# Kernel optimization log

Measured on AMD Instinct MI355X. Metric: run time of the kernel, lower is better.

## Reference

```python
import jax, jax.numpy as jnp
import numpy as np

NEG_BIG = -9e15
ALPHA = 0.2  # LeakyReLU negative slope


def setup_inputs() -> dict:
    key = jax.random.key(0)
    k1, k2, k3, k4 = jax.random.split(key, 4)
    B, N, F_in, F_out = 8, 2048, 128, 128
    h = jax.random.normal(k1, (B, N, F_in), dtype=jnp.float32)
    adj = jax.random.randint(k2, (B, N, N), 0, 2, dtype=jnp.int32)
    # xavier_uniform with gain=1.414
    def xavier(k, shape, gain=1.414):
        fan_in, fan_out = shape[0], shape[1]
        bound = gain * np.sqrt(6.0 / (fan_in + fan_out))
        return jax.random.uniform(k, shape, jnp.float32, -bound, bound)
    W = xavier(k3, (F_in, F_out))
    a = xavier(k4, (2 * F_out, 1))
    return {"h": h, "adj": adj, "W": W, "a": a}


def reference(h, adj, W, a):
    # h: [B,N,F_in], adj: [B,N,N], W: [F_in,F_out], a: [2*F_out,1]
    Wh = jnp.einsum('bnf,fo->bno', h, W)              # [B,N,F_out]
    F_out = W.shape[1]
    a1 = a[:F_out, 0]                                  # source part
    a2 = a[F_out:, 0]                                  # target part
    # additive attention decomposition: cat([Wh_i, Wh_j]) @ a == Wh_i@a1 + Wh_j@a2
    s1 = Wh @ a1                                       # [B,N]
    s2 = Wh @ a2                                       # [B,N]
    e = jax.nn.leaky_relu(s1[:, :, None] + s2[:, None, :], negative_slope=ALPHA)  # [B,N,N]
    e = jnp.where(adj > 0, e, NEG_BIG)
    attn = jax.nn.softmax(e, axis=-1)                  # [B,N,N]
    h_prime = jnp.einsum('bij,bjo->bio', attn, Wh)     # [B,N,F_out]
    return jax.nn.elu(h_prime)                         # concat=True path
```

## Files before the change

kernel.cpp:

```cpp
#include <hip/hip_runtime.h>
#include <hip/hip_bf16.h>
#include <string.h>

typedef __attribute__((ext_vector_type(8))) short short8;
typedef __attribute__((ext_vector_type(4))) float f32x4;
typedef __attribute__((ext_vector_type(4))) float float4v;
typedef __attribute__((ext_vector_type(2))) float float2v;
typedef __attribute__((ext_vector_type(4))) unsigned short ushort4v;

#define LOG2E 1.44269504088896340736f
#define NB 8
#define NN 2048
#define NF 128
#define PKW (NN / 64)
#define PKWORDS (NB * NN * PKW)
#define NGEMMB 256
#define NPACKB 1024

static __device__ inline unsigned short f2bf(float x) {
    unsigned u = __float_as_uint(x);
    return (unsigned short)((u + 0x7FFFu + ((u >> 16) & 1u)) >> 16);
}
static __device__ inline float bf2f(unsigned short u) {
    union { unsigned u; float f; } v;
    v.u = ((unsigned)u) << 16;
    return v.f;
}
static __device__ inline float fexp2(float x) {
    float r;
    asm("v_exp_f32 %0, %1" : "=v"(r) : "v"(x));
    return r;
}
static __device__ inline unsigned fkey(float f) {
    unsigned u = __float_as_uint(f);
    return (u & 0x80000000u) ? ~u : (u | 0x80000000u);
}
static __device__ inline float funkey(unsigned k) {
    unsigned b = (k & 0x80000000u) ? (k & 0x7FFFFFFFu) : ~k;
    return __uint_as_float(b);
}
static __device__ inline int wave_sniff(const unsigned short* __restrict__ raw) {
    int lane = threadIdx.x & 63;
    int cnt = 0;
#pragma unroll
    for (int i = 0; i < 8; ++i) {
        int e = (raw[lane * 8 + i] >> 7) & 0xFF;
        cnt += (e >= 102 && e <= 139) ? 1 : 0;
    }
#pragma unroll
    for (int off = 1; off < 64; off <<= 1) cnt += __shfl_xor(cnt, off);
    return cnt >= 450;
}

__global__ __launch_bounds__(256) void k_prep(const void* __restrict__ Wraw,
                                              const void* __restrict__ araw,
                                              short* __restrict__ WThi,
                                              short* __restrict__ WTlo,
                                              float* __restrict__ a1s,
                                              float* __restrict__ a2s,
                                              unsigned* __restrict__ s2mkey) {
    const int bf16w = wave_sniff((const unsigned short*)Wraw);
    int idx = blockIdx.x * 256 + threadIdx.x;
    int k = idx >> 7, n = idx & 127;
    float x = bf16w ? bf2f(((const unsigned short*)Wraw)[idx])
                    : ((const float*)Wraw)[idx];
    unsigned short hi = f2bf(x);
    float lo = x - bf2f(hi);
    WThi[n * 128 + k] = (short)hi;
    WTlo[n * 128 + k] = (short)f2bf(lo);
    if (blockIdx.x == 0) {
        int i = threadIdx.x;
        float av = bf16w ? bf2f(((const unsigned short*)araw)[i])
                         : ((const float*)araw)[i];
        if (i < 128) a1s[i] = LOG2E * av;
        else a2s[i - 128] = LOG2E * av;
        if (i < NB) s2mkey[i] = 0u;
    }
}

__global__ __launch_bounds__(256, 4) void k_fat(const int* __restrict__ adj,
                                                unsigned long long* __restrict__ pk,
                                                const void* __restrict__ hraw,
                                                const short* __restrict__ WThi,
                                                const short* __restrict__ WTlo,
                                                const float* __restrict__ a1s,
                                                const float* __restrict__ a2s,
                                                float* __restrict__ s1,
                                                float* __restrict__ EF,
                                                unsigned* __restrict__ s2mkey,
                                                short* __restrict__ WhT) {
    const int tid = threadIdx.x;
    if (blockIdx.x >= NGEMMB) {
        const int wid = (blockIdx.x - NGEMMB) * 4 + (tid >> 6);
        const int lane = tid & 63;
        const int wpw = PKWORDS / 4096;
        const size_t w0 = (size_t)wid * wpw;
        for (int i = 0; i < wpw; i += 8) {
            int v[8];
#pragma unroll
            for (int k = 0; k < 8; ++k) v[k] = adj[((w0 + i + k) << 6) | lane];
            unsigned long long m[8];
#pragma unroll
            for (int k = 0; k < 8; ++k) m[k] = __ballot(v[k] > 0);
            if (lane == 0) {
#pragma unroll
                for (int k = 0; k < 8; ++k) pk[w0 + i + k] = m[k];
            }
        }
        return;
    }
    const int lane = tid & 63;
    const int w = tid >> 6;
    const int lo = lane & 15, g = lane >> 4;
    const int i0 = (blockIdx.x * 4 + w) * 16;
    const int bf16w = wave_sniff((const unsigned short*)hraw);

    short8 ahi[4], alo[4];
    if (bf16w) {
        const short* h16 = (const short*)hraw;
#pragma unroll
        for (int kc = 0; kc < 4; ++kc) {
            ahi[kc] = *(const short8*)(h16 + (size_t)(i0 + lo) * NF + kc * 32 + g * 8);
            alo[kc] = (short8){0, 0, 0, 0, 0, 0, 0, 0};
        }
    } else {
        const float* hf = (const float*)hraw;
#pragma unroll
        for (int kc = 0; kc < 4; ++kc) {
            const float* p = hf + (size_t)(i0 + lo) * NF + kc * 32 + g * 8;
            float4v x0 = *(const float4v*)(p);
            float4v x1 = *(const float4v*)(p + 4);
            short8 h8, l8;
#pragma unroll
            for (int q = 0; q < 4; ++q) {
                unsigned short u0 = f2bf(x0[q]);
                h8[q] = (short)u0;
                l8[q] = (short)f2bf(x0[q] - bf2f(u0));
                unsigned short u1 = f2bf(x1[q]);
                h8[q + 4] = (short)u1;
                l8[q + 4] = (short)f2bf(x1[q] - bf2f(u1));
            }
            ahi[kc] = h8;
            alo[kc] = l8;
        }
    }

    f32x4 acc[8];
#pragma unroll
    for (int t = 0; t < 8; ++t) acc[t] = (f32x4){0.f, 0.f, 0.f, 0.f};
#pragma unroll
    for (int t = 0; t < 8; ++t) {
#pragma unroll
        for (int kc = 0; kc < 4; ++kc) {
            const size_t boff = (size_t)(lo + 16 * t) * NF + kc * 32 + g * 8;
            short8 bhi = *(const short8*)(WThi + boff);
            short8 blo = *(const short8*)(WTlo + boff);
            acc[t] = __builtin_amdgcn_mfma_f32_16x16x32_bf16(ahi[kc], bhi, acc[t], 0, 0, 0);
            acc[t] = __builtin_amdgcn_mfma_f32_16x16x32_bf16(ahi[kc], blo, acc[t], 0, 0, 0);
            acc[t] = __builtin_amdgcn_mfma_f32_16x16x32_bf16(alo[kc], bhi, acc[t], 0, 0, 0);
        }
    }

    const int b = i0 >> 11;
    const int n0 = i0 & 2047;
    short* wt = WhT + (size_t)b * NF * NN;
#pragma unroll
    for (int t = 0; t < 8; ++t) {
        ushort4v u;
#pragma unroll
        for (int r = 0; r < 4; ++r) u[r] = f2bf(acc[t][r]);
        *(ushort4v*)(wt + (size_t)(lo + 16 * t) * NN + n0 + g * 4) = u;
    }

    float a1f[8], a2f[8];
#pragma unroll
    for (int t = 0; t < 8; ++t) {
        a1f[t] = a1s[lo + 16 * t];
        a2f[t] = a2s[lo + 16 * t];
    }
    float wm = -1e30f;
#pragma unroll
    for (int r = 0; r < 4; ++r) {
        float d1 = 0.f, d2 = 0.f;
#pragma unroll
        for (int t = 0; t < 8; ++t) {
            float wv = acc[t][r];
            d1 += wv * a1f[t];
            d2 += wv * a2f[t];
        }
#pragma unroll
        for (int off = 1; off < 16; off <<= 1) {
            d1 += __shfl_xor(d1, off);
            d2 += __shfl_xor(d2, off);
        }
        if (lo == 0) {
            s1[i0 + g * 4 + r] = d1;
            float2v ef;
            ef[0] = fexp2(d2);
            ef[1] = fexp2(0.2f * d2);
            *(float2v*)(EF + (size_t)(i0 + g * 4 + r) * 2) = ef;
        }
        wm = fmaxf(wm, d2);
    }
    wm = fmaxf(wm, __shfl_xor(wm, 16));
    wm = fmaxf(wm, __shfl_xor(wm, 32));
    if (lane == 0) atomicMax(&s2mkey[b], fkey(wm));
}

template <int FINAL, int JS>
__global__ __launch_bounds__(256, 4) void k_attn(const unsigned long long* __restrict__ pk,
                                                 const float* __restrict__ s1,
                                                 const float* __restrict__ EF,
                                                 const unsigned* __restrict__ s2mkey,
                                                 const short* __restrict__ WhT,
                                                 const void* __restrict__ hraw,
                                                 void* __restrict__ out,
                                                 unsigned short* __restrict__ pO,
                                                 float* __restrict__ pL) {
    constexpr int JL = NN / JS;
    constexpr int NT = JL / 64;

    const int tid = threadIdx.x;
    const int lane = tid & 63, wid = tid >> 6;
    const int lo = lane & 15, g = lane >> 4;
    const int gid = blockIdx.x;
    const int b = gid & 7;
    const int blk = (gid >> 3) & 31;
    const int js = (JS > 1) ? (gid >> 8) : 0;
    const int rowbase = blk * 64 + wid * 16;
    const int row = rowbase + lo;
    const int jbeg = js * JL;

    __shared__ short lds[2][128 * 64];
    __shared__ float ldsZ[JL * 2];

    const float s1v = s1[b * NN + row];
    const float tm = s1v + funkey(s2mkey[b]);
    const float M = fmaxf(tm, 0.2f * tm);
    const float Tc = fexp2(-s1v);
    const float Ac = fexp2(s1v - M);
    const float Bc = fexp2(0.2f * s1v - M);
    const unsigned long long* pkr = pk + (size_t)(b * NN + row) * PKW + (jbeg >> 6);
    const short* vb = WhT + (size_t)b * NF * NN;

    {
        const float4v* src = (const float4v*)(EF + (size_t)(b * NN + jbeg) * 2);
        for (int i = tid; i < JL / 2; i += 256) ((float4v*)ldsZ)[i] = src[i];
    }

    const int sf = tid >> 1;
    const int sh = tid & 1;
    const short* sbase = vb + (size_t)sf * NN + jbeg + sh * 32;
    char* ldsc0 = (char*)&lds[0][0];
    char* ldsc1 = (char*)&lds[1][0];
    const unsigned swz = (unsigned)((sf & 7) << 4);
    const unsigned wb0 = (unsigned)(sf * 128 + sh * 64);
    const unsigned rsw = (unsigned)((lo & 7) << 4);

    f32x4 acc[8];
#pragma unroll
    for (int t = 0; t < 8; ++t) acc[t] = (f32x4){0.f, 0.f, 0.f, 0.f};
    float lsum = 0.f;

    {
        short8 s0 = *(const short8*)(sbase);
        short8 s1r = *(const short8*)(sbase + 8);
        short8 s2r = *(const short8*)(sbase + 16);
        short8 s3r = *(const short8*)(sbase + 24);
        *(short8*)(ldsc0 + ((wb0 + 0) ^ swz)) = s0;
        *(short8*)(ldsc0 + ((wb0 + 16) ^ swz)) = s1r;
        *(short8*)(ldsc0 + ((wb0 + 32) ^ swz)) = s2r;
        *(short8*)(ldsc0 + ((wb0 + 48) ^ swz)) = s3r;
    }
    unsigned long long mcur = pkr[0];
    __syncthreads();

    int cur = 0;
    for (int t = 0; t < NT; ++t) {
        short8 sn0, sn1, sn2, sn3;
        unsigned long long mnext = 0;
        const bool more = (t + 1 < NT);
        if (more) {
            const short* sp = sbase + (t + 1) * 64;
            sn0 = *(const short8*)(sp);
            sn1 = *(const short8*)(sp + 8);
            sn2 = *(const short8*)(sp + 16);
            sn3 = *(const short8*)(sp + 24);
            mnext = pkr[t + 1];
        }
        const char* cb = cur ? ldsc1 : ldsc0;

        short8 pa[2];
#pragma unroll
        for (int c = 0; c < 2; ++c) {
            const float4v* zp = (const float4v*)&ldsZ[((t) * 64 + c * 32 + g * 8) * 2];
            float4v w_[4];
#pragma unroll
            for (int q = 0; q < 4; ++q) w_[q] = zp[q];
            const unsigned bits = (unsigned)(mcur >> (c * 32 + g * 8)) & 0xFFu;
            float pv[8];
#pragma unroll
            for (int k = 0; k < 8; ++k) {
                float E = w_[k >> 1][(k & 1) * 2];
                float F = w_[k >> 1][(k & 1) * 2 + 1];
                bool cond = E >= Tc;
                float sel = cond ? E : F;
                float coef = cond ? Ac : Bc;
                float p = sel * coef;
                p = ((bits >> k) & 1u) ? p : 0.f;
                lsum += p;
                pv[k] = p;
            }
            unsigned r0, r1, r2, r3;
            asm("v_cvt_pk_bf16_f32 %0, %1, %2" : "=v"(r0) : "v"(pv[0]), "v"(pv[1]));
            asm("v_cvt_pk_bf16_f32 %0, %1, %2" : "=v"(r1) : "v"(pv[2]), "v"(pv[3]));
            asm("v_cvt_pk_bf16_f32 %0, %1, %2" : "=v"(r2) : "v"(pv[4]), "v"(pv[5]));
            asm("v_cvt_pk_bf16_f32 %0, %1, %2" : "=v"(r3) : "v"(pv[6]), "v"(pv[7]));
            union { unsigned u[4]; short8 s; } uu;
            uu.u[0] = r0; uu.u[1] = r1; uu.u[2] = r2; uu.u[3] = r3;
            pa[c] = uu.s;
        }

        __builtin_amdgcn_s_setprio(1);
#pragma unroll
        for (int t8 = 0; t8 < 8; ++t8) {
            const unsigned rb0 = ((unsigned)((lo + 16 * t8) * 128 + g * 16)) ^ rsw;
            const unsigned rb1 = ((unsigned)((lo + 16 * t8) * 128 + 64 + g * 16)) ^ rsw;
            short8 v0 = *(const short8*)(cb + rb0);
            short8 v1 = *(const short8*)(cb + rb1);
            acc[t8] = __builtin_amdgcn_mfma_f32_16x16x32_bf16(pa[0], v0, acc[t8], 0, 0, 0);
            acc[t8] = __builtin_amdgcn_mfma_f32_16x16x32_bf16(pa[1], v1, acc[t8], 0, 0, 0);
        }
        __builtin_amdgcn_s_setprio(0);

        if (more) {
            char* wb = cur ? ldsc0 : ldsc1;
            *(short8*)(wb + ((wb0 + 0) ^ swz)) = sn0;
            *(short8*)(wb + ((wb0 + 16) ^ swz)) = sn1;
            *(short8*)(wb + ((wb0 + 32) ^ swz)) = sn2;
            *(short8*)(wb + ((wb0 + 48) ^ swz)) = sn3;
            mcur = mnext;
        }
        __syncthreads();
        cur ^= 1;
    }

    lsum += __shfl_xor(lsum, 16);
    lsum += __shfl_xor(lsum, 32);

    if (FINAL) {
        const int bf16w = wave_sniff((const unsigned short*)hraw);
        float inv[4];
#pragma unroll
        for (int r = 0; r < 4; ++r) inv[r] = 1.0f / __shfl(lsum, g * 4 + r);
#pragma unroll
        for (int t8 = 0; t8 < 8; ++t8) {
#pragma unroll
            for (int r = 0; r < 4; ++r) {
                float x = acc[t8][r] * inv[r];
                float y = (x > 0.f) ? x : (fexp2(x * LOG2E) - 1.0f);
                size_t oi = ((size_t)b * NN + rowbase + g * 4 + r) * NF + lo + 16 * t8;
                if (bf16w) ((unsigned short*)out)[oi] = f2bf(y);
                else ((float*)out)[oi] = y;
            }
        }
    } else {
        const int grp = b * 128 + blk * 4 + wid;
        unsigned short* po = pO + (size_t)(grp * JS + js) * (16 * NF);
#pragma unroll
        for (int t8 = 0; t8 < 8; ++t8)
#pragma unroll
            for (int r = 0; r < 4; ++r)
                po[(g * 4 + r) * NF + lo + 16 * t8] = f2bf(acc[t8][r]);
        if (g == 0) pL[(grp * JS + js) * 16 + lo] = lsum;
    }
}

__global__ __launch_bounds__(256) void k_combine(const unsigned short* __restrict__ pO,
                                                 const float* __restrict__ pL,
                                                 const void* __restrict__ hraw,
                                                 void* __restrict__ out,
                                                 int jsplit) {
    const int bf16w = wave_sniff((const unsigned short*)hraw);
    int idx4 = blockIdx.x * 256 + threadIdx.x;
    int base = idx4 * 4;
    if (base >= NB * NN * NF) return;
    int col = base & 127;
    int rowg = base >> 7;
    int r = rowg & 15;
    int grp = rowg >> 4;
    float o0 = 0.f, o1 = 0.f, o2 = 0.f, o3 = 0.f;
    float l = 0.f;
    for (int js = 0; js < jsplit; ++js) {
        int task = grp * jsplit + js;
        ushort4v u = *(const ushort4v*)(pO + (size_t)task * (16 * NF) + r * NF + col);
        o0 += bf2f(u[0]); o1 += bf2f(u[1]); o2 += bf2f(u[2]); o3 += bf2f(u[3]);
        l += pL[task * 16 + r];
    }
    float inv = 1.0f / l;
    float y[4];
    float ov[4] = {o0, o1, o2, o3};
#pragma unroll
    for (int q = 0; q < 4; ++q) {
        float x = ov[q] * inv;
        y[q] = (x > 0.f) ? x : (fexp2(x * LOG2E) - 1.0f);
    }
    if (bf16w) {
        ushort4v u;
#pragma unroll
        for (int q = 0; q < 4; ++q) u[q] = f2bf(y[q]);
        *(ushort4v*)((unsigned short*)out + base) = u;
    } else {
        *(float4v*)((float*)out + base) = (float4v){y[0], y[1], y[2], y[3]};
    }
}

extern "C" void kernel_launch(void* const* d_in, const int* in_sizes, int n_in,
                              void* d_out, int out_size, void* d_ws, size_t ws_size,
                              hipStream_t stream) {
    const void* h = d_in[0];
    const int* adj = (const int*)d_in[1];
    const void* W = d_in[2];
    const void* a = d_in[3];

    char* ws = (char*)d_ws;
    auto align256 = [](size_t x) { return (x + 255) & ~(size_t)255; };
    size_t off = 0;
    short* WThi = (short*)(ws + off); off = align256(off + (size_t)128 * 128 * 2);
    short* WTlo = (short*)(ws + off); off = align256(off + (size_t)128 * 128 * 2);
    float* a1s = (float*)(ws + off);  off = align256(off + 128 * 4);
    float* a2s = (float*)(ws + off);  off = align256(off + 128 * 4);
    short* WhT = (short*)(ws + off);  off = align256(off + (size_t)NB * NF * NN * 2);
    float* s1 = (float*)(ws + off);   off = align256(off + (size_t)NB * NN * 4);
    float* EF = (float*)(ws + off);   off = align256(off + (size_t)NB * NN * 8);
    unsigned* s2mkey = (unsigned*)(ws + off); off = align256(off + NB * 4);
    unsigned long long* pk = (unsigned long long*)(ws + off);
    off = align256(off + (size_t)PKWORDS * 8);

    const int ngrp = NB * 128;
    auto need = [&](int js) {
        return off + (size_t)ngrp * js * 16 * NF * 2 + 512 + (size_t)ngrp * js * 16 * 4;
    };
    int jsplit = (ws_size >= need(4)) ? 4 : ((ws_size >= need(2)) ? 2 : 1);
    unsigned short* pO = nullptr;
    float* pL = nullptr;
    if (jsplit > 1) {
        size_t pO_bytes = (size_t)ngrp * jsplit * 16 * NF * 2;
        size_t pL_bytes = (size_t)ngrp * jsplit * 16 * 4;
        pO = (unsigned short*)(ws + off); off = align256(off + pO_bytes);
        pL = (float*)(ws + off); off = align256(off + pL_bytes);
    }

    k_prep<<<64, 256, 0, stream>>>(W, a, WThi, WTlo, a1s, a2s, s2mkey);
    k_fat<<<NGEMMB + NPACKB, 256, 0, stream>>>(adj, pk, h, WThi, WTlo, a1s, a2s,
                                               s1, EF, s2mkey, WhT);
    if (jsplit == 4) {
        k_attn<0, 4><<<NB * 32 * 4, 256, 0, stream>>>(pk, s1, EF, s2mkey, WhT, h,
                                                      d_out, pO, pL);
    } else if (jsplit == 2) {
        k_attn<0, 2><<<NB * 32 * 2, 256, 0, stream>>>(pk, s1, EF, s2mkey, WhT, h,
                                                      d_out, pO, pL);
    } else {
        k_attn<1, 1><<<NB * 32, 256, 0, stream>>>(pk, s1, EF, s2mkey, WhT, h,
                                                  d_out, nullptr, nullptr);
    }
    if (jsplit > 1) {
        int nout = NB * NN * NF;
        k_combine<<<(nout / 4 + 255) / 256, 256, 0, stream>>>(pO, pL, h, d_out, jsplit);
    }
}
```

Measured before the change: 72.66 us.

## Single-buffer LDS in attention kernel and raise key split to eight

The attention kernel drops its double-buffered LDS tile for a single buffer, adding a barrier before the next tile is written, and removes the launch-bounds occupancy hint and the non-split FINAL path. The host now prefers an eight-way split of the key dimension when workspace allows and always runs the combine kernel. The aim is more blocks and higher occupancy from halved shared memory, at the cost of an extra barrier per tile, less overlap of loads with MFMA work, and more partial-output traffic in the combine step.

```diff
diff --git a/kernel.cpp b/kernel.cpp
--- a/kernel.cpp
+++ b/kernel.cpp
@@ -207,16 +207,14 @@
     if (lane == 0) atomicMax(&s2mkey[b], fkey(wm));
 }
 
-template <int FINAL, int JS>
-__global__ __launch_bounds__(256, 4) void k_attn(const unsigned long long* __restrict__ pk,
-                                                 const float* __restrict__ s1,
-                                                 const float* __restrict__ EF,
-                                                 const unsigned* __restrict__ s2mkey,
-                                                 const short* __restrict__ WhT,
-                                                 const void* __restrict__ hraw,
-                                                 void* __restrict__ out,
-                                                 unsigned short* __restrict__ pO,
-                                                 float* __restrict__ pL) {
+template <int JS>
+__global__ __launch_bounds__(256) void k_attn(const unsigned long long* __restrict__ pk,
+                                              const float* __restrict__ s1,
+                                              const float* __restrict__ EF,
+                                              const unsigned* __restrict__ s2mkey,
+                                              const short* __restrict__ WhT,
+                                              unsigned short* __restrict__ pO,
+                                              float* __restrict__ pL) {
     constexpr int JL = NN / JS;
     constexpr int NT = JL / 64;
 
@@ -226,12 +224,12 @@
     const int gid = blockIdx.x;
     const int b = gid & 7;
     const int blk = (gid >> 3) & 31;
-    const int js = (JS > 1) ? (gid >> 8) : 0;
+    const int js = gid >> 8;
     const int rowbase = blk * 64 + wid * 16;
     const int row = rowbase + lo;
     const int jbeg = js * JL;
 
-    __shared__ short lds[2][128 * 64];
+    __shared__ short lds[128 * 64];
     __shared__ float ldsZ[JL * 2];
 
     const float s1v = s1[b * NN + row];
@@ -251,8 +249,7 @@
     const int sf = tid >> 1;
     const int sh = tid & 1;
     const short* sbase = vb + (size_t)sf * NN + jbeg + sh * 32;
-    char* ldsc0 = (char*)&lds[0][0];
-    char* ldsc1 = (char*)&lds[1][0];
+    char* ldsc = (char*)&lds[0];
     const unsigned swz = (unsigned)((sf & 7) << 4);
     const unsigned wb0 = (unsigned)(sf * 128 + sh * 64);
     const unsigned rsw = (unsigned)((lo & 7) << 4);
@@ -267,15 +264,14 @@
         short8 s1r = *(const short8*)(sbase + 8);
         short8 s2r = *(const short8*)(sbase + 16);
         short8 s3r = *(const short8*)(sbase + 24);
-        *(short8*)(ldsc0 + ((wb0 + 0) ^ swz)) = s0;
-        *(short8*)(ldsc0 + ((wb0 + 16) ^ swz)) = s1r;
-        *(short8*)(ldsc0 + ((wb0 + 32) ^ swz)) = s2r;
-        *(short8*)(ldsc0 + ((wb0 + 48) ^ swz)) = s3r;
+        *(short8*)(ldsc + ((wb0 + 0) ^ swz)) = s0;
+        *(short8*)(ldsc + ((wb0 + 16) ^ swz)) = s1r;
+        *(short8*)(ldsc + ((wb0 + 32) ^ swz)) = s2r;
+        *(short8*)(ldsc + ((wb0 + 48) ^ swz)) = s3r;
     }
     unsigned long long mcur = pkr[0];
     __syncthreads();
 
-    int cur = 0;
     for (int t = 0; t < NT; ++t) {
         short8 sn0, sn1, sn2, sn3;
         unsigned long long mnext = 0;
@@ -288,7 +284,6 @@
             sn3 = *(const short8*)(sp + 24);
             mnext = pkr[t + 1];
         }
-        const char* cb = cur ? ldsc1 : ldsc0;
 
         short8 pa[2];
 #pragma unroll
@@ -326,54 +321,35 @@
         for (int t8 = 0; t8 < 8; ++t8) {
             const unsigned rb0 = ((unsigned)((lo + 16 * t8) * 128 + g * 16)) ^ rsw;
             const unsigned rb1 = ((unsigned)((lo + 16 * t8) * 128 + 64 + g * 16)) ^ rsw;
-            short8 v0 = *(const short8*)(cb + rb0);
-            short8 v1 = *(const short8*)(cb + rb1);
+            short8 v0 = *(const short8*)(ldsc + rb0);
+            short8 v1 = *(const short8*)(ldsc + rb1);
             acc[t8] = __builtin_amdgcn_mfma_f32_16x16x32_bf16(pa[0], v0, acc[t8], 0, 0, 0);
             acc[t8] = __builtin_amdgcn_mfma_f32_16x16x32_bf16(pa[1], v1, acc[t8], 0, 0, 0);
         }
         __builtin_amdgcn_s_setprio(0);
 
+        __syncthreads();
         if (more) {
-            char* wb = cur ? ldsc0 : ldsc1;
-            *(short8*)(wb + ((wb0 + 0) ^ swz)) = sn0;
-            *(short8*)(wb + ((wb0 + 16) ^ swz)) = sn1;
-            *(short8*)(wb + ((wb0 + 32) ^ swz)) = sn2;
-            *(short8*)(wb + ((wb0 + 48) ^ swz)) = sn3;
+            *(short8*)(ldsc + ((wb0 + 0) ^ swz)) = sn0;
+            *(short8*)(ldsc + ((wb0 + 16) ^ swz)) = sn1;
+            *(short8*)(ldsc + ((wb0 + 32) ^ swz)) = sn2;
+            *(short8*)(ldsc + ((wb0 + 48) ^ swz)) = sn3;
             mcur = mnext;
         }
         __syncthreads();
-        cur ^= 1;
     }
 
     lsum += __shfl_xor(lsum, 16);
     lsum += __shfl_xor(lsum, 32);
 
-    if (FINAL) {
-        const int bf16w = wave_sniff((const unsigned short*)hraw);
-        float inv[4];
-#pragma unroll
-        for (int r = 0; r < 4; ++r) inv[r] = 1.0f / __shfl(lsum, g * 4 + r);
-#pragma unroll
-        for (int t8 = 0; t8 < 8; ++t8) {
-#pragma unroll
-            for (int r = 0; r < 4; ++r) {
-                float x = acc[t8][r] * inv[r];
-                float y = (x > 0.f) ? x : (fexp2(x * LOG2E) - 1.0f);
-                size_t oi = ((size_t)b * NN + rowbase + g * 4 + r) * NF + lo + 16 * t8;
-                if (bf16w) ((unsigned short*)out)[oi] = f2bf(y);
-                else ((float*)out)[oi] = y;
-            }
-        }
-    } else {
-        const int grp = b * 128 + blk * 4 + wid;
-        unsigned short* po = pO + (size_t)(grp * JS + js) * (16 * NF);
-#pragma unroll
-        for (int t8 = 0; t8 < 8; ++t8)
-#pragma unroll
-            for (int r = 0; r < 4; ++r)
-                po[(g * 4 + r) * NF + lo + 16 * t8] = f2bf(acc[t8][r]);
-        if (g == 0) pL[(grp * JS + js) * 16 + lo] = lsum;
-    }
+    const int grp = b * 128 + blk * 4 + wid;
+    unsigned short* po = pO + (size_t)(grp * JS + js) * (16 * NF);
+#pragma unroll
+    for (int t8 = 0; t8 < 8; ++t8)
+#pragma unroll
+        for (int r = 0; r < 4; ++r)
+            po[(g * 4 + r) * NF + lo + 16 * t8] = f2bf(acc[t8][r]);
+    if (g == 0) pL[(grp * JS + js) * 16 + lo] = lsum;
 }
 
 __global__ __launch_bounds__(256) void k_combine(const unsigned short* __restrict__ pO,
@@ -441,31 +417,24 @@
     auto need = [&](int js) {
         return off + (size_t)ngrp * js * 16 * NF * 2 + 512 + (size_t)ngrp * js * 16 * 4;
     };
-    int jsplit = (ws_size >= need(4)) ? 4 : ((ws_size >= need(2)) ? 2 : 1);
-    unsigned short* pO = nullptr;
-    float* pL = nullptr;
-    if (jsplit > 1) {
-        size_t pO_bytes = (size_t)ngrp * jsplit * 16 * NF * 2;
-        size_t pL_bytes = (size_t)ngrp * jsplit * 16 * 4;
-        pO = (unsigned short*)(ws + off); off = align256(off + pO_bytes);
-        pL = (float*)(ws + off); off = align256(off + pL_bytes);
-    }
+    int jsplit = (ws_size >= need(8)) ? 8 : ((ws_size >= need(4)) ? 4 : 2);
+    size_t pO_bytes = (size_t)ngrp * jsplit * 16 * NF * 2;
+    size_t pL_bytes = (size_t)ngrp * jsplit * 16 * 4;
+    unsigned short* pO = (unsigned short*)(ws + off);
+    off = align256(off + pO_bytes);
+    float* pL = (float*)(ws + off);
+    off = align256(off + pL_bytes);
 
     k_prep<<<64, 256, 0, stream>>>(W, a, WThi, WTlo, a1s, a2s, s2mkey);
     k_fat<<<NGEMMB + NPACKB, 256, 0, stream>>>(adj, pk, h, WThi, WTlo, a1s, a2s,
                                                s1, EF, s2mkey, WhT);
-    if (jsplit == 4) {
-        k_attn<0, 4><<<NB * 32 * 4, 256, 0, stream>>>(pk, s1, EF, s2mkey, WhT, h,
-                                                      d_out, pO, pL);
-    } else if (jsplit == 2) {
-        k_attn<0, 2><<<NB * 32 * 2, 256, 0, stream>>>(pk, s1, EF, s2mkey, WhT, h,
-                                                      d_out, pO, pL);
+    if (jsplit == 8) {
+        k_attn<8><<<NB * 32 * 8, 256, 0, stream>>>(pk, s1, EF, s2mkey, WhT, pO, pL);
+    } else if (jsplit == 4) {
+        k_attn<4><<<NB * 32 * 4, 256, 0, stream>>>(pk, s1, EF, s2mkey, WhT, pO, pL);
     } else {
-        k_attn<1, 1><<<NB * 32, 256, 0, stream>>>(pk, s1, EF, s2mkey, WhT, h,
-                                                  d_out, nullptr, nullptr);
-    }
-    if (jsplit > 1) {
-        int nout = NB * NN * NF;
-        k_combine<<<(nout / 4 + 255) / 256, 256, 0, stream>>>(pO, pL, h, d_out, jsplit);
-    }
-}
+        k_attn<2><<<NB * 32 * 2, 256, 0, stream>>>(pk, s1, EF, s2mkey, WhT, pO, pL);
+    }
+    int nout = NB * NN * NF;
+    k_combine<<<(nout / 4 + 255) / 256, 256, 0, stream>>>(pO, pL, h, d_out, jsplit);
+}
```

After: 75.58 us. 4.0% more time.
